# Kernel optimization log

Measured on AMD Instinct MI355X. Metric: run time of the kernel, lower is better.

Reference implementation:

```python
import jax, jax.numpy as jnp
import numpy as np

HIDDEN_DIM = 2048
LAYER_IDX = 12
NUM_LAYERS = 24
BATCH, SEQ_LEN = 4, 4096

def _init_time_decay(layer_idx, num_layers, hidden_dim):
    ratio = layer_idx / max(num_layers - 1, 1)
    i = np.arange(hidden_dim, dtype=np.float32)
    channel_ratio = i / max(hidden_dim - 1, 1)
    zigzag = ((i + 1) % 3 - 1) * 0.1
    decay = -5 + 4.5 * (ratio * 0.3 + channel_ratio * 0.7) + zigzag
    return jnp.asarray(decay, dtype=jnp.float32)

def setup_inputs() -> dict:
    key = jax.random.key(0)
    k1, k2 = jax.random.split(key)
    k = jax.random.normal(k1, (BATCH, SEQ_LEN, HIDDEN_DIM), dtype=jnp.float32)
    v = jax.random.normal(k2, (BATCH, SEQ_LEN, HIDDEN_DIM), dtype=jnp.float32)
    time_decay = _init_time_decay(LAYER_IDX, NUM_LAYERS, HIDDEN_DIM)
    time_first = jnp.zeros((HIDDEN_DIM,), dtype=jnp.float32)
    return {"k": k, "v": v, "time_decay": time_decay, "time_first": time_first}

def reference(k, v, time_decay, time_first):
    # w = -exp(time_decay); per-step decay factor ew = exp(w)
    ew = jnp.exp(-jnp.exp(time_decay))          # (H,)
    u = time_first                              # (H,)
    eps = 1e-8

    # scan over time: carry (a, b) each (B, H)
    def step(carry, kv_t):
        a, b = carry
        k_t, v_t = kv_t                         # (B, H) each
        ek = jnp.exp(k_t)
        euk = jnp.exp(u + k_t)
        wkv_t = (a + euk * v_t) / (b + euk + eps)
        new_a = ew * a + ek * v_t
        new_b = ew * b + ek
        return (new_a, new_b), wkv_t

    B, T, H = k.shape
    a0 = jnp.zeros((B, H), dtype=k.dtype)
    b0 = jnp.zeros((B, H), dtype=k.dtype)
    # time-major for scan
    kT = jnp.transpose(k, (1, 0, 2))            # (T, B, H)
    vT = jnp.transpose(v, (1, 0, 2))
    (a, b), outT = jax.lax.scan(step, (a0, b0), (kT, vT))
    output = jnp.transpose(outT, (1, 0, 2))     # (B, T, H)
    return output, a, b
```

## Files before the change

### kernel.cpp

```cpp
#include <hip/hip_runtime.h>
#include <math.h>
#include <stdint.h>

#define B 4
#define T 4096
#define H 2048
#define TT 256
#define NT (T / TT)
#define NBAND (H / 32)
#define THREADS 1024
#define NSUB 32
#define SUBL (TT / NSUB)

typedef const __attribute__((address_space(1))) uint32_t* gas_ptr;
typedef __attribute__((address_space(3))) uint32_t* las_ptr;

__device__ __forceinline__ void stage8(const float* gbase, float* lbase, int lane) {
    __builtin_amdgcn_global_load_lds(
        (gas_ptr)(const void*)(gbase + (lane >> 3) * H + (lane & 7) * 4),
        (las_ptr)(void*)lbase, 16, 0, 0);
}

__global__ __launch_bounds__(THREADS)
void wkv_fused_kernel(const float* __restrict__ kg,
                      const float* __restrict__ vg,
                      const float* __restrict__ td,
                      const float* __restrict__ tf,
                      float* __restrict__ out) {
    __shared__ float  lk[2][TT][32];
    __shared__ float  lv[2][TT][32];
    __shared__ float2 sab[2][NSUB][32];

    int band = blockIdx.x & (NBAND - 1);
    int b    = blockIdx.x >> 6;
    int tid  = threadIdx.x;
    int lane = tid & 63;
    int wv   = tid >> 6;
    int ch   = tid & 31;
    int sub  = tid >> 5;

    const float* kbase = kg + (size_t)b * T * H + band * 32;
    const float* vbase = vg + (size_t)b * T * H + band * 32;
    float* obase       = out + (size_t)b * T * H + band * 32;

    int h = band * 32 + ch;
    float ew = expf(-expf(td[h]));
    float eu = expf(tf[h]);

    float e2 = ew * ew, e4 = e2 * e2;
    float ewL  = e4 * e4;
    float l2   = ewL * ewL;
    float l4   = l2 * l2;
    float l8   = l4 * l4;
    float l16  = l8 * l8;
    float ewT  = l16 * l16;
    float ewpow = 1.0f;
    if (sub & 1)  ewpow *= ewL;
    if (sub & 2)  ewpow *= l2;
    if (sub & 4)  ewpow *= l4;
    if (sub & 8)  ewpow *= l8;
    if (sub & 16) ewpow *= l16;

    float Ra = 0.f, Rb = 0.f;

#define ISSUE(tile, bufi)                                                   \
    {                                                                       \
        _Pragma("unroll")                                                   \
        for (int ii = 0; ii < 2; ++ii) {                                    \
            int g = wv * 2 + ii;                                            \
            stage8(kbase + ((size_t)(tile) * TT + 8 * g) * H,               \
                   &lk[bufi][8 * g][0], lane);                              \
            stage8(vbase + ((size_t)(tile) * TT + 8 * g) * H,               \
                   &lv[bufi][8 * g][0], lane);                              \
        }                                                                   \
    }

    ISSUE(0, 0);
    for (int j = 0; j < NT; ++j) {
        const int cur = j & 1;
        if (j + 1 < NT) ISSUE(j + 1, cur ^ 1);
        if (j == 0) {
            asm volatile("s_waitcnt vmcnt(4)" ::: "memory");
        } else if (j + 1 < NT) {
            asm volatile("s_waitcnt vmcnt(12)" ::: "memory");
        } else {
            asm volatile("s_waitcnt vmcnt(8)" ::: "memory");
        }

        float ek[SUBL], ekv[SUBL];
        float la = 0.f, lb = 0.f;
#pragma unroll
        for (int i = 0; i < SUBL; ++i) {
            int t = sub * SUBL + i;
            float kk = lk[cur][t][ch];
            float vv = lv[cur][t][ch];
            float e  = __expf(kk);
            float ev = e * vv;
            ek[i]  = e;
            ekv[i] = ev;
            la = ew * la + ev;
            lb = ew * lb + e;
        }
        sab[cur][sub][ch] = make_float2(la, lb);
        asm volatile("s_waitcnt lgkmcnt(0)" ::: "memory");
        __builtin_amdgcn_s_barrier();

        float ta = 0.f, tb = 0.f, pa = 0.f, pb = 0.f;
#pragma unroll
        for (int s = 0; s < NSUB; ++s) {
            float2 x = sab[cur][s][ch];
            bool cap = (s == sub);
            pa = cap ? ta : pa;
            pb = cap ? tb : pb;
            ta = ewL * ta + x.x;
            tb = ewL * tb + x.y;
        }
        float a2 = ewpow * Ra + pa;
        float b2 = ewpow * Rb + pb;
        Ra = ewT * Ra + ta;
        Rb = ewT * Rb + tb;

#pragma unroll
        for (int i = 0; i < SUBL; ++i) {
            int t = sub * SUBL + i;
            float num = a2 + eu * ekv[i];
            float den = b2 + eu * ek[i] + 1e-8f;
            float inv;
            asm("v_rcp_f32 %0, %1" : "=v"(inv) : "v"(den));
            float r = num * inv;
            __builtin_nontemporal_store(r, obase + ((size_t)j * TT + t) * H + ch);
            a2 = ew * a2 + ekv[i];
            b2 = ew * b2 + ek[i];
        }
    }

    if (tid < 32) {
        size_t so = (size_t)B * T * H;
        out[so + (size_t)b * H + h] = Ra;
        out[so + (size_t)B * H + (size_t)b * H + h] = Rb;
    }
}

extern "C" void kernel_launch(void* const* d_in, const int* in_sizes, int n_in,
                              void* d_out, int out_size, void* d_ws, size_t ws_size,
                              hipStream_t stream) {
    const float* k  = (const float*)d_in[0];
    const float* v  = (const float*)d_in[1];
    const float* td = (const float*)d_in[2];
    const float* tf = (const float*)d_in[3];
    float* out      = (float*)d_out;

    dim3 grid(B * NBAND);
    wkv_fused_kernel<<<grid, dim3(THREADS), 0, stream>>>(k, v, td, tf, out);
}
```

Measured before the change: 74.30 us.

## Replace LDS staging with direct per-thread register prefetch of k/v tiles

Removes the global_load_lds staging into shared-memory double buffers. Each thread now loads its own 8 k/v values straight into registers, with a register double buffer that prefetches the next tile, and the tile loop is unrolled by two to swap the buffers. This drops the LDS traffic and the hand-written vmcnt waits, and frees a large amount of shared memory. In exchange the global loads become 128-byte row segments per half-wave instead of 16-byte vector loads, and register pressure rises at 1024 threads per block.

Result: faster. 70.08 us (-5.7%).

```diff
diff --git a/kernel.cpp b/kernel.cpp
--- a/kernel.cpp
+++ b/kernel.cpp
@@ -1,6 +1,5 @@
 #include <hip/hip_runtime.h>
 #include <math.h>
-#include <stdint.h>
 
 #define B 4
 #define T 4096
@@ -12,36 +11,23 @@
 #define NSUB 32
 #define SUBL (TT / NSUB)
 
-typedef const __attribute__((address_space(1))) uint32_t* gas_ptr;
-typedef __attribute__((address_space(3))) uint32_t* las_ptr;
-
-__device__ __forceinline__ void stage8(const float* gbase, float* lbase, int lane) {
-    __builtin_amdgcn_global_load_lds(
-        (gas_ptr)(const void*)(gbase + (lane >> 3) * H + (lane & 7) * 4),
-        (las_ptr)(void*)lbase, 16, 0, 0);
-}
-
 __global__ __launch_bounds__(THREADS)
 void wkv_fused_kernel(const float* __restrict__ kg,
                       const float* __restrict__ vg,
                       const float* __restrict__ td,
                       const float* __restrict__ tf,
                       float* __restrict__ out) {
-    __shared__ float  lk[2][TT][32];
-    __shared__ float  lv[2][TT][32];
     __shared__ float2 sab[2][NSUB][32];
 
     int band = blockIdx.x & (NBAND - 1);
     int b    = blockIdx.x >> 6;
     int tid  = threadIdx.x;
-    int lane = tid & 63;
-    int wv   = tid >> 6;
     int ch   = tid & 31;
     int sub  = tid >> 5;
 
-    const float* kbase = kg + (size_t)b * T * H + band * 32;
-    const float* vbase = vg + (size_t)b * T * H + band * 32;
-    float* obase       = out + (size_t)b * T * H + band * 32;
+    const float* kbase = kg + (size_t)b * T * H + band * 32 + ch;
+    const float* vbase = vg + (size_t)b * T * H + band * 32 + ch;
+    float* obase       = out + (size_t)b * T * H + band * 32 + ch;
 
     int h = band * 32 + ch;
     float ew = expf(-expf(td[h]));
@@ -63,75 +49,73 @@
 
     float Ra = 0.f, Rb = 0.f;
 
-#define ISSUE(tile, bufi)                                                   \
+    const size_t rbase = (size_t)sub * SUBL * H;
+
+#define LOADTILE(J, KN, VN)                                                 \
     {                                                                       \
         _Pragma("unroll")                                                   \
-        for (int ii = 0; ii < 2; ++ii) {                                    \
-            int g = wv * 2 + ii;                                            \
-            stage8(kbase + ((size_t)(tile) * TT + 8 * g) * H,               \
-                   &lk[bufi][8 * g][0], lane);                              \
-            stage8(vbase + ((size_t)(tile) * TT + 8 * g) * H,               \
-                   &lv[bufi][8 * g][0], lane);                              \
+        for (int i = 0; i < SUBL; ++i) {                                    \
+            size_t off = (size_t)(J) * TT * H + rbase + (size_t)i * H;      \
+            KN[i] = kbase[off];                                             \
+            VN[i] = vbase[off];                                             \
         }                                                                   \
     }
 
-    ISSUE(0, 0);
-    for (int j = 0; j < NT; ++j) {
-        const int cur = j & 1;
-        if (j + 1 < NT) ISSUE(j + 1, cur ^ 1);
-        if (j == 0) {
-            asm volatile("s_waitcnt vmcnt(4)" ::: "memory");
-        } else if (j + 1 < NT) {
-            asm volatile("s_waitcnt vmcnt(12)" ::: "memory");
-        } else {
-            asm volatile("s_waitcnt vmcnt(8)" ::: "memory");
-        }
+#define TILE_BODY(J, KC, VC, KN, VN)                                        \
+    {                                                                       \
+        const int cur = (J) & 1;                                            \
+        if ((J) + 1 < NT) LOADTILE((J) + 1, KN, VN);                        \
+           \
+        float ek[SUBL], ekv[SUBL];                                          \
+        float la = 0.f, lb = 0.f;                                           \
+        _Pragma("unroll")                                                   \
+        for (int i = 0; i < SUBL; ++i) {                                    \
+            float e  = __expf(KC[i]);                                       \
+            float ev = e * VC[i];                                           \
+            ek[i]  = e;                                                     \
+            ekv[i] = ev;                                                    \
+            la = ew * la + ev;                                              \
+            lb = ew * lb + e;                                               \
+        }                                                                   \
+        sab[cur][sub][ch] = make_float2(la, lb);                            \
+        asm volatile("s_waitcnt lgkmcnt(0)" ::: "memory");                  \
+        __builtin_amdgcn_s_barrier();            \
+         \
+        float ta = 0.f, tb = 0.f, pa = 0.f, pb = 0.f;                       \
+        _Pragma("unroll")                                                   \
+        for (int s = 0; s < NSUB; ++s) {                                    \
+            float2 x = sab[cur][s][ch];                                     \
+            bool cap = (s == sub);                                          \
+            pa = cap ? ta : pa;                                             \
+            pb = cap ? tb : pb;                                             \
+            ta = ewL * ta + x.x;                                            \
+            tb = ewL * tb + x.y;                                            \
+        }                                                                   \
+        float a2 = ewpow * Ra + pa;                                         \
+        float b2 = ewpow * Rb + pb;                                         \
+        Ra = ewT * Ra + ta;                                                 \
+        Rb = ewT * Rb + tb;                                                 \
+                                 \
+        _Pragma("unroll")                                                   \
+        for (int i = 0; i < SUBL; ++i) {                                    \
+            float num = a2 + eu * ekv[i];                                   \
+            float den = b2 + eu * ek[i] + 1e-8f;                            \
+            float inv;                                                      \
+            asm("v_rcp_f32 %0, %1" : "=v"(inv) : "v"(den));                 \
+            float r = num * inv;                                            \
+            __builtin_nontemporal_store(                                    \
+                r, obase + (size_t)(J) * TT * H + rbase + (size_t)i * H);   \
+            a2 = ew * a2 + ekv[i];                                          \
+            b2 = ew * b2 + ek[i];                                           \
+        }                                                                   \
+    }
 
-        float ek[SUBL], ekv[SUBL];
-        float la = 0.f, lb = 0.f;
-#pragma unroll
-        for (int i = 0; i < SUBL; ++i) {
-            int t = sub * SUBL + i;
-            float kk = lk[cur][t][ch];
-            float vv = lv[cur][t][ch];
-            float e  = __expf(kk);
-            float ev = e * vv;
-            ek[i]  = e;
-            ekv[i] = ev;
-            la = ew * la + ev;
-            lb = ew * lb + e;
-        }
-        sab[cur][sub][ch] = make_float2(la, lb);
-        asm volatile("s_waitcnt lgkmcnt(0)" ::: "memory");
-        __builtin_amdgcn_s_barrier();
+    float ka[SUBL], va[SUBL], kb2[SUBL], vb2[SUBL];
+    LOADTILE(0, ka, va);
 
-        float ta = 0.f, tb = 0.f, pa = 0.f, pb = 0.f;
-#pragma unroll
-        for (int s = 0; s < NSUB; ++s) {
-            float2 x = sab[cur][s][ch];
-            bool cap = (s == sub);
-            pa = cap ? ta : pa;
-            pb = cap ? tb : pb;
-            ta = ewL * ta + x.x;
-            tb = ewL * tb + x.y;
-        }
-        float a2 = ewpow * Ra + pa;
-        float b2 = ewpow * Rb + pb;
-        Ra = ewT * Ra + ta;
-        Rb = ewT * Rb + tb;
-
-#pragma unroll
-        for (int i = 0; i < SUBL; ++i) {
-            int t = sub * SUBL + i;
-            float num = a2 + eu * ekv[i];
-            float den = b2 + eu * ek[i] + 1e-8f;
-            float inv;
-            asm("v_rcp_f32 %0, %1" : "=v"(inv) : "v"(den));
-            float r = num * inv;
-            __builtin_nontemporal_store(r, obase + ((size_t)j * TT + t) * H + ch);
-            a2 = ew * a2 + ekv[i];
-            b2 = ew * b2 + ek[i];
-        }
+    for (int j = 0; j < NT; j += 2) {
+        TILE_BODY(j,     ka,  va,  kb2, vb2);
+        TILE_BODY(j + 1, kb2, vb2, ka,  va);
     }
 
     if (tid < 32) {
```
